# Kernel tuning notes

Measured on AMD Instinct MI355X. Metric: run time of the kernel, lower is better.

The kernel has to match this reference:

```python
import jax, jax.numpy as jnp
import numpy as np

D_MODEL = 512
INF = 1e9
TEMP = np.sqrt(D_MODEL).astype(np.float32)


def setup_inputs() -> dict:
    key = jax.random.key(0)
    kq, kk, kv, km = jax.random.split(key, 4)
    B, L, D = 64, 1024, 64  # B = batch*heads
    q = jax.random.normal(kq, (B, L, D), dtype=jnp.float32)
    k = jax.random.normal(kk, (B, L, D), dtype=jnp.float32)
    v = jax.random.normal(kv, (B, L, D), dtype=jnp.float32)
    attn_mask = jax.random.randint(km, (B, L, L), 0, 2).astype(jnp.bool_)
    return {"q": q, "k": k, "v": v, "attn_mask": attn_mask}


def reference(q, k, v, attn_mask):
    # scores: [b, len_q, len_k]
    attn = jnp.einsum('bqd,bkd->bqk', q, k) / TEMP
    attn = jnp.where(attn_mask, -INF, attn)
    attn = jax.nn.softmax(attn, axis=2)
    # dropout p=0.0 -> identity
    out = jnp.einsum('bqk,bkd->bqd', attn, v)
    return out
```

## Files before the change

kernel.cpp:

```cpp
#include <hip/hip_runtime.h>
#include <hip/hip_bf16.h>


typedef __attribute__((ext_vector_type(4))) float f32x4;
typedef __attribute__((ext_vector_type(8))) short bf16x8;
typedef __attribute__((ext_vector_type(4))) short short4v;

constexpr int B_ = 64;
constexpr int L_ = 1024;
constexpr int D_ = 64;
constexpr int QBLK = 64;
constexpr int KV = 64;
constexpr int NT_H = 8;
constexpr int STR = 72;
constexpr float SC2 = 0.06376003f;
constexpr float NEG = -1e9f;
constexpr float THR = 8.0f;

constexpr int HBUF = 64 * STR * 2;

__device__ inline short f2bf(float f) {
  __hip_bfloat16 h = __float2bfloat16(f);
  short s; __builtin_memcpy(&s, &h, 2);
  return s;
}
__device__ inline unsigned int pk2(float a, float b) {
  return (unsigned int)(unsigned short)f2bf(a)
       | ((unsigned int)(unsigned short)f2bf(b) << 16);
}

__global__ __launch_bounds__(512, 4) void attn_fwd(
    const float* __restrict__ Q, const float* __restrict__ K,
    const float* __restrict__ V, const int* __restrict__ M,
    float* __restrict__ O)
{
  __shared__ __align__(16) unsigned char smem[4 * HBUF + 512];

  const int tid  = threadIdx.x;
  const int w    = tid >> 6;
  const int half = w >> 2;
  const int w4   = w & 3;
  const int lane = tid & 63;
  const int g    = lane >> 4;
  const int c    = lane & 15;
  const int htid = tid & 255;
  const int b    = blockIdx.y;
  const int q0   = blockIdx.x * QBLK;

  short (*k_lds)[STR]  = (short(*)[STR])(smem + half * (2 * HBUF));
  short (*vt_lds)[STR] = (short(*)[STR])(smem + half * (2 * HBUF) + HBUF);

  bf16x8 qf[2];
  {
    const float* qp = Q + ((size_t)b * L_ + q0 + w4 * 16 + c) * D_ + g * 8;
#pragma unroll
    for (int ks = 0; ks < 2; ++ks) {
      f32x4 x0 = *(const f32x4*)(qp + ks * 32);
      f32x4 x1 = *(const f32x4*)(qp + ks * 32 + 4);
      bf16x8 t;
      t[0] = f2bf(x0[0]); t[1] = f2bf(x0[1]); t[2] = f2bf(x0[2]); t[3] = f2bf(x0[3]);
      t[4] = f2bf(x1[0]); t[5] = f2bf(x1[1]); t[6] = f2bf(x1[2]); t[7] = f2bf(x1[3]);
      qf[ks] = t;
    }
  }

  const float* Kb = K + (size_t)b * L_ * D_ + (size_t)half * NT_H * KV * D_;
  const float* Vb = V + (size_t)b * L_ * D_ + (size_t)half * NT_H * KV * D_;
  const int* mlane = M + (size_t)b * L_ * L_
                   + (size_t)(q0 + w4 * 16 + c) * L_ + half * (NT_H * KV) + 4 * g;

  const int vkey4 = (htid & 15) * 4;
  const int vd4   = (htid >> 4) * 4;

  auto stage = [&](int t) {
    const float* ksrc = Kb + (size_t)(t * KV) * D_;
    const float* vsrc = Vb + (size_t)(t * KV) * D_;
#pragma unroll
    for (int i = 0; i < 4; ++i) {
      const int idx = htid + i * 256;
      f32x4 kx = *(const f32x4*)(ksrc + (size_t)idx * 4);
      short4v ks4 = { f2bf(kx[0]), f2bf(kx[1]), f2bf(kx[2]), f2bf(kx[3]) };
      *(short4v*)&k_lds[idx >> 4][(idx & 15) * 4] = ks4;
    }
    f32x4 vreg[4];
#pragma unroll
    for (int i = 0; i < 4; ++i)
      vreg[i] = *(const f32x4*)(vsrc + (size_t)(vkey4 + i) * D_ + vd4);
#pragma unroll
    for (int i = 0; i < 4; ++i) {
      const int jj = (i + (htid >> 4)) & 3;
      short4v vt4 = { f2bf(vreg[0][jj]), f2bf(vreg[1][jj]),
                      f2bf(vreg[2][jj]), f2bf(vreg[3][jj]) };
      *(short4v*)&vt_lds[vd4 + jj][vkey4] = vt4;
    }
  };

  f32x4 acc[4];
#pragma unroll
  for (int i = 0; i < 4; ++i) acc[i] = (f32x4){0.f, 0.f, 0.f, 0.f};
  float m_run = -INFINITY;
  float l_run = 0.f;

  stage(0);
  __syncthreads();

  for (int t = 0; t < NT_H; ++t) {
    unsigned int mc = 0;
#pragma unroll
    for (int f = 0; f < 4; ++f) {
      const int4 lm = *(const int4*)(mlane + t * KV + f * 16);
      mc |= (lm.x != 0 ? 1u : 0u) << (f * 4 + 0);
      mc |= (lm.y != 0 ? 1u : 0u) << (f * 4 + 1);
      mc |= (lm.z != 0 ? 1u : 0u) << (f * 4 + 2);
      mc |= (lm.w != 0 ? 1u : 0u) << (f * 4 + 3);
    }

    f32x4 sc[4];
#pragma unroll
    for (int f = 0; f < 4; ++f) {
      f32x4 a = (f32x4){0.f, 0.f, 0.f, 0.f};
#pragma unroll
      for (int ks = 0; ks < 2; ++ks) {
        bf16x8 kf = *(const bf16x8*)&k_lds[f * 16 + c][ks * 32 + g * 8];
        a = __builtin_amdgcn_mfma_f32_16x16x32_bf16(kf, qf[ks], a, 0, 0, 0);
      }
      sc[f] = a;
    }

#pragma unroll
    for (int f = 0; f < 4; ++f)
#pragma unroll
      for (int r = 0; r < 4; ++r)
        sc[f][r] = ((mc >> (f * 4 + r)) & 1u) ? NEG : sc[f][r] * SC2;

    float xl = sc[0][0];
#pragma unroll
    for (int f = 0; f < 4; ++f)
#pragma unroll
      for (int r = 0; r < 4; ++r) xl = fmaxf(xl, sc[f][r]);
    if (!__all(xl <= m_run + THR)) {
      float x = fmaxf(xl, __shfl_xor(xl, 16, 64));
      x = fmaxf(x, __shfl_xor(x, 32, 64));
      const float m_new = fmaxf(m_run, x);
      const float alpha = exp2f(m_run - m_new);
      l_run *= alpha;
      float ar[4];
#pragma unroll
      for (int r = 0; r < 4; ++r)
        ar[r] = __shfl(alpha, (lane & 48) | (g * 4 + r), 64);
#pragma unroll
      for (int fd = 0; fd < 4; ++fd)
#pragma unroll
        for (int r = 0; r < 4; ++r) acc[fd][r] *= ar[r];
      m_run = m_new;
    }
    float s = 0.f;
#pragma unroll
    for (int f = 0; f < 4; ++f)
#pragma unroll
      for (int r = 0; r < 4; ++r) {
        const float p = exp2f(sc[f][r] - m_run);
        sc[f][r] = p;
        s += p;
      }
    l_run += s;

    unsigned int pd[4][2];
#pragma unroll
    for (int f = 0; f < 4; ++f) {
      pd[f][0] = pk2(sc[f][0], sc[f][1]);
      pd[f][1] = pk2(sc[f][2], sc[f][3]);
    }
    const int rev2 = ((g & 1) << 1) | (g >> 1);
    const int srcA = rev2 * 16 + c;
    const int srcB = srcA ^ 16;
    const bool podd = (g & 1) != 0;
    const bool gh   = (g >= 2);
    unsigned int d0[4], d1[4];
#pragma unroll
    for (int k = 0; k < 4; ++k) {
      const int fb = 2 * (k >> 1);
      const int hh = k & 1;
      const unsigned int pubA = podd ? pd[fb + 1][hh] : pd[fb + 0][hh];
      const unsigned int pubB = podd ? pd[fb + 0][hh] : pd[fb + 1][hh];
      const unsigned int rvA = (unsigned int)__shfl((int)pubA, srcA, 64);
      const unsigned int rvB = (unsigned int)__shfl((int)pubB, srcB, 64);
      if (k < 2) {
        if (gh) { d0[2 + hh] = rvA; d0[hh] = rvB; }
        else    { d0[hh] = rvA; d0[2 + hh] = rvB; }
      } else {
        if (gh) { d1[2 + hh] = rvA; d1[hh] = rvB; }
        else    { d1[hh] = rvA; d1[2 + hh] = rvB; }
      }
    }
    bf16x8 pa0, pa1;
    __builtin_memcpy(&pa0, d0, 16);
    __builtin_memcpy(&pa1, d1, 16);

#pragma unroll
    for (int fd = 0; fd < 4; ++fd) {
      bf16x8 vb0 = *(const bf16x8*)&vt_lds[fd * 16 + c][g * 8];
      acc[fd] = __builtin_amdgcn_mfma_f32_16x16x32_bf16(pa0, vb0, acc[fd], 0, 0, 0);
      bf16x8 vb1 = *(const bf16x8*)&vt_lds[fd * 16 + c][32 + g * 8];
      acc[fd] = __builtin_amdgcn_mfma_f32_16x16x32_bf16(pa1, vb1, acc[fd], 0, 0, 0);
    }

    if (t + 1 < NT_H) {
      __syncthreads();
      stage(t + 1);
      __syncthreads();
    }
  }

  float l = l_run;
  l += __shfl_xor(l, 16, 64);
  l += __shfl_xor(l, 32, 64);

  __syncthreads();
  f32x4* cacc = (f32x4*)smem;
  float2* cml = (float2*)(smem + 4 * HBUF);
  if (half == 1) {
#pragma unroll
    for (int fd = 0; fd < 4; ++fd)
      cacc[(w4 * 64 + lane) * 4 + fd] = acc[fd];
    if (g == 0) cml[w4 * 16 + c] = make_float2(m_run, l);
  }
  __syncthreads();
  if (half == 0) {
    const float2 mlB = cml[w4 * 16 + c];
    const float Mx = fmaxf(m_run, mlB.x);
    const float wA = exp2f(m_run - Mx);
    const float wB = exp2f(mlB.x - Mx);
    const float li = 1.0f / (wA * l + wB * mlB.y);
    float arA[4], arB[4], lr[4];
#pragma unroll
    for (int r = 0; r < 4; ++r) {
      const int src = (lane & 48) | (g * 4 + r);
      arA[r] = __shfl(wA, src, 64);
      arB[r] = __shfl(wB, src, 64);
      lr[r]  = __shfl(li, src, 64);
    }
    float* orow = O + ((size_t)b * L_ + q0 + w4 * 16 + g * 4) * D_;
#pragma unroll
    for (int fd = 0; fd < 4; ++fd) {
      const f32x4 ab = cacc[(w4 * 64 + lane) * 4 + fd];
#pragma unroll
      for (int r = 0; r < 4; ++r)
        orow[(size_t)r * D_ + fd * 16 + c] =
            (arA[r] * acc[fd][r] + arB[r] * ab[r]) * lr[r];
    }
  }
}

extern "C" void kernel_launch(void* const* d_in, const int* in_sizes, int n_in,
                              void* d_out, int out_size, void* d_ws, size_t ws_size,
                              hipStream_t stream) {
  const float* q = (const float*)d_in[0];
  const float* k = (const float*)d_in[1];
  const float* v = (const float*)d_in[2];
  const int* m = (const int*)d_in[3];
  float* o = (float*)d_out;
  dim3 grid(L_ / QBLK, B_);
  attn_fwd<<<grid, 512, 0, stream>>>(q, k, v, m, o);
}
```

Before: 117.2 us.

## Double-buffer K/V in LDS and prefetch tiles and mask into registers

Doubles the LDS buffers so each half-block loads the next K/V tile from global into registers before computing the current tile, then writes it to the alternate buffer. This removes one barrier per iteration. Mask loads are prefetched two tiles ahead, and the loop is unrolled by two so the mask registers can alternate. In exchange, LDS usage doubles, register pressure grows, and the occupancy hint in launch bounds drops from 4 to 2 blocks, which may reduce latency hiding across waves.

```diff
diff --git a/kernel.cpp b/kernel.cpp
--- a/kernel.cpp
+++ b/kernel.cpp
@@ -17,7 +17,8 @@
 constexpr float NEG = -1e9f;
 constexpr float THR = 8.0f;
 
-constexpr int HBUF = 64 * STR * 2;
+constexpr int HBUF    = 64 * STR * 2;
+constexpr int HALFREG = 4 * HBUF;
 
 __device__ inline short f2bf(float f) {
   __hip_bfloat16 h = __float2bfloat16(f);
@@ -29,12 +30,12 @@
        | ((unsigned int)(unsigned short)f2bf(b) << 16);
 }
 
-__global__ __launch_bounds__(512, 4) void attn_fwd(
+__global__ __launch_bounds__(512, 2) void attn_fwd(
     const float* __restrict__ Q, const float* __restrict__ K,
     const float* __restrict__ V, const int* __restrict__ M,
     float* __restrict__ O)
 {
-  __shared__ __align__(16) unsigned char smem[4 * HBUF + 512];
+  __shared__ __align__(16) unsigned char smem[2 * HALFREG + 512];
 
   const int tid  = threadIdx.x;
   const int w    = tid >> 6;
@@ -47,8 +48,12 @@
   const int b    = blockIdx.y;
   const int q0   = blockIdx.x * QBLK;
 
-  short (*k_lds)[STR]  = (short(*)[STR])(smem + half * (2 * HBUF));
-  short (*vt_lds)[STR] = (short(*)[STR])(smem + half * (2 * HBUF) + HBUF);
+  auto k_base  = [&](int buf) {
+    return (short(*)[STR])(smem + half * HALFREG + buf * (2 * HBUF));
+  };
+  auto vt_base = [&](int buf) {
+    return (short(*)[STR])(smem + half * HALFREG + buf * (2 * HBUF) + HBUF);
+  };
 
   bf16x8 qf[2];
   {
@@ -72,27 +77,48 @@
   const int vkey4 = (htid & 15) * 4;
   const int vd4   = (htid >> 4) * 4;
 
-  auto stage = [&](int t) {
+  f32x4 kreg[4], vreg[4];
+  int4  mr0[4], mr1[4];
+
+  auto load_kv = [&](int t) {
     const float* ksrc = Kb + (size_t)(t * KV) * D_;
     const float* vsrc = Vb + (size_t)(t * KV) * D_;
 #pragma unroll
     for (int i = 0; i < 4; ++i) {
+      kreg[i] = *(const f32x4*)(ksrc + (size_t)(htid + i * 256) * 4);
+      vreg[i] = *(const f32x4*)(vsrc + (size_t)(vkey4 + i) * D_ + vd4);
+    }
+  };
+  auto load_m = [&](int t, int4 (&mr)[4]) {
+#pragma unroll
+    for (int f = 0; f < 4; ++f)
+      mr[f] = *(const int4*)(mlane + t * KV + f * 16);
+  };
+  auto write_kv = [&](int buf) {
+    short (*kl)[STR]  = k_base(buf);
+    short (*vtl)[STR] = vt_base(buf);
+#pragma unroll
+    for (int i = 0; i < 4; ++i) {
       const int idx = htid + i * 256;
-      f32x4 kx = *(const f32x4*)(ksrc + (size_t)idx * 4);
-      short4v ks4 = { f2bf(kx[0]), f2bf(kx[1]), f2bf(kx[2]), f2bf(kx[3]) };
-      *(short4v*)&k_lds[idx >> 4][(idx & 15) * 4] = ks4;
-    }
-    f32x4 vreg[4];
-#pragma unroll
-    for (int i = 0; i < 4; ++i)
-      vreg[i] = *(const f32x4*)(vsrc + (size_t)(vkey4 + i) * D_ + vd4);
-#pragma unroll
-    for (int i = 0; i < 4; ++i) {
+      short4v ks4 = { f2bf(kreg[i][0]), f2bf(kreg[i][1]),
+                      f2bf(kreg[i][2]), f2bf(kreg[i][3]) };
+      *(short4v*)&kl[idx >> 4][(idx & 15) * 4] = ks4;
       const int jj = (i + (htid >> 4)) & 3;
       short4v vt4 = { f2bf(vreg[0][jj]), f2bf(vreg[1][jj]),
                       f2bf(vreg[2][jj]), f2bf(vreg[3][jj]) };
-      *(short4v*)&vt_lds[vd4 + jj][vkey4] = vt4;
-    }
+      *(short4v*)&vtl[vd4 + jj][vkey4] = vt4;
+    }
+  };
+  auto packm = [&](const int4 (&lm)[4]) {
+    unsigned int mp = 0;
+#pragma unroll
+    for (int f = 0; f < 4; ++f) {
+      mp |= (lm[f].x != 0 ? 1u : 0u) << (f * 4 + 0);
+      mp |= (lm[f].y != 0 ? 1u : 0u) << (f * 4 + 1);
+      mp |= (lm[f].z != 0 ? 1u : 0u) << (f * 4 + 2);
+      mp |= (lm[f].w != 0 ? 1u : 0u) << (f * 4 + 3);
+    }
+    return mp;
   };
 
   f32x4 acc[4];
@@ -101,27 +127,30 @@
   float m_run = -INFINITY;
   float l_run = 0.f;
 
-  stage(0);
+  load_kv(0);
+  write_kv(0);
+  load_m(0, mr0);
+  load_m(1, mr1);
+  __builtin_amdgcn_sched_barrier(0);
   __syncthreads();
 
-  for (int t = 0; t < NT_H; ++t) {
-    unsigned int mc = 0;
-#pragma unroll
-    for (int f = 0; f < 4; ++f) {
-      const int4 lm = *(const int4*)(mlane + t * KV + f * 16);
-      mc |= (lm.x != 0 ? 1u : 0u) << (f * 4 + 0);
-      mc |= (lm.y != 0 ? 1u : 0u) << (f * 4 + 1);
-      mc |= (lm.z != 0 ? 1u : 0u) << (f * 4 + 2);
-      mc |= (lm.w != 0 ? 1u : 0u) << (f * 4 + 3);
-    }
-
+  auto body = [&](int t, int4 (&mr)[4]) {
+    const int cur = t & 1;
+    const bool has_next = (t + 1 < NT_H);
+    if (has_next) load_kv(t + 1);
+    const unsigned int mc = packm(mr);
+    if (t + 2 < NT_H) load_m(t + 2, mr);
+    __builtin_amdgcn_sched_barrier(0);
+
+    short (*kl)[STR]  = k_base(cur);
+    short (*vtl)[STR] = vt_base(cur);
     f32x4 sc[4];
 #pragma unroll
     for (int f = 0; f < 4; ++f) {
       f32x4 a = (f32x4){0.f, 0.f, 0.f, 0.f};
 #pragma unroll
       for (int ks = 0; ks < 2; ++ks) {
-        bf16x8 kf = *(const bf16x8*)&k_lds[f * 16 + c][ks * 32 + g * 8];
+        bf16x8 kf = *(const bf16x8*)&kl[f * 16 + c][ks * 32 + g * 8];
         a = __builtin_amdgcn_mfma_f32_16x16x32_bf16(kf, qf[ks], a, 0, 0, 0);
       }
       sc[f] = a;
@@ -199,17 +228,21 @@
 
 #pragma unroll
     for (int fd = 0; fd < 4; ++fd) {
-      bf16x8 vb0 = *(const bf16x8*)&vt_lds[fd * 16 + c][g * 8];
+      bf16x8 vb0 = *(const bf16x8*)&vtl[fd * 16 + c][g * 8];
       acc[fd] = __builtin_amdgcn_mfma_f32_16x16x32_bf16(pa0, vb0, acc[fd], 0, 0, 0);
-      bf16x8 vb1 = *(const bf16x8*)&vt_lds[fd * 16 + c][32 + g * 8];
+      bf16x8 vb1 = *(const bf16x8*)&vtl[fd * 16 + c][32 + g * 8];
       acc[fd] = __builtin_amdgcn_mfma_f32_16x16x32_bf16(pa1, vb1, acc[fd], 0, 0, 0);
     }
 
-    if (t + 1 < NT_H) {
+    if (has_next) {
+      write_kv(cur ^ 1);
       __syncthreads();
-      stage(t + 1);
-      __syncthreads();
-    }
+    }
+  };
+
+  for (int tt = 0; tt < NT_H; tt += 2) {
+    body(tt,     mr0);
+    body(tt + 1, mr1);
   }
 
   float l = l_run;
@@ -218,7 +251,7 @@
 
   __syncthreads();
   f32x4* cacc = (f32x4*)smem;
-  float2* cml = (float2*)(smem + 4 * HBUF);
+  float2* cml = (float2*)(smem + 2 * HALFREG);
   if (half == 1) {
 #pragma unroll
     for (int fd = 0; fd < 4; ++fd)
```

New measurement: 175.4 us. +49.7%, slower.

## Prefetch next K/V tile and mask into registers to overlap with compute

Applied to the files above, without the earlier changes.

Splits staging into global load, bf16 conversion and LDS write, and issues the loads for tile t+1 (K, V and the mask) at the start of iteration t. The global latency is then hidden behind the QK MFMAs and softmax instead of sitting between barriers. Scheduling barriers pin the load placement. Launch bounds drop from 4 to 2 blocks per SM to make room for the extra live registers, which may cut occupancy.

```diff
diff --git a/kernel.cpp b/kernel.cpp
--- a/kernel.cpp
+++ b/kernel.cpp
@@ -17,7 +17,8 @@
 constexpr float NEG = -1e9f;
 constexpr float THR = 8.0f;
 
-constexpr int HBUF = 64 * STR * 2;
+constexpr int HBUF     = 64 * STR * 2;
+constexpr int HALF_LDS = 2 * HBUF;
 
 __device__ inline short f2bf(float f) {
   __hip_bfloat16 h = __float2bfloat16(f);
@@ -29,12 +30,12 @@
        | ((unsigned int)(unsigned short)f2bf(b) << 16);
 }
 
-__global__ __launch_bounds__(512, 4) void attn_fwd(
+__global__ __launch_bounds__(512, 2) void attn_fwd(
     const float* __restrict__ Q, const float* __restrict__ K,
     const float* __restrict__ V, const int* __restrict__ M,
     float* __restrict__ O)
 {
-  __shared__ __align__(16) unsigned char smem[4 * HBUF + 512];
+  __shared__ __align__(16) unsigned char smem[2 * HALF_LDS + 512];
 
   const int tid  = threadIdx.x;
   const int w    = tid >> 6;
@@ -47,8 +48,8 @@
   const int b    = blockIdx.y;
   const int q0   = blockIdx.x * QBLK;
 
-  short (*k_lds)[STR]  = (short(*)[STR])(smem + half * (2 * HBUF));
-  short (*vt_lds)[STR] = (short(*)[STR])(smem + half * (2 * HBUF) + HBUF);
+  short (*k_lds)[STR]  = (short(*)[STR])(smem + half * HALF_LDS);
+  short (*vt_lds)[STR] = (short(*)[STR])(smem + half * HALF_LDS + HBUF);
 
   bf16x8 qf[2];
   {
@@ -72,26 +73,41 @@
   const int vkey4 = (htid & 15) * 4;
   const int vd4   = (htid >> 4) * 4;
 
-  auto stage = [&](int t) {
+  f32x4   kreg[4], vreg[4];
+  short4v ksh[4], vsh[4];
+  int4    mr[4];
+
+  auto load_kv = [&](int t) {
     const float* ksrc = Kb + (size_t)(t * KV) * D_;
     const float* vsrc = Vb + (size_t)(t * KV) * D_;
 #pragma unroll
     for (int i = 0; i < 4; ++i) {
+      kreg[i] = *(const f32x4*)(ksrc + (size_t)(htid + i * 256) * 4);
+      vreg[i] = *(const f32x4*)(vsrc + (size_t)(vkey4 + i) * D_ + vd4);
+    }
+  };
+  auto load_m = [&](int t) {
+#pragma unroll
+    for (int f = 0; f < 4; ++f)
+      mr[f] = *(const int4*)(mlane + t * KV + f * 16);
+  };
+  auto cvt_kv = [&]() {
+#pragma unroll
+    for (int i = 0; i < 4; ++i) {
+      ksh[i] = short4v{ f2bf(kreg[i][0]), f2bf(kreg[i][1]),
+                        f2bf(kreg[i][2]), f2bf(kreg[i][3]) };
+      const int jj = (i + (htid >> 4)) & 3;
+      vsh[i] = short4v{ f2bf(vreg[0][jj]), f2bf(vreg[1][jj]),
+                        f2bf(vreg[2][jj]), f2bf(vreg[3][jj]) };
+    }
+  };
+  auto write_kv = [&]() {
+#pragma unroll
+    for (int i = 0; i < 4; ++i) {
       const int idx = htid + i * 256;
-      f32x4 kx = *(const f32x4*)(ksrc + (size_t)idx * 4);
-      short4v ks4 = { f2bf(kx[0]), f2bf(kx[1]), f2bf(kx[2]), f2bf(kx[3]) };
-      *(short4v*)&k_lds[idx >> 4][(idx & 15) * 4] = ks4;
-    }
-    f32x4 vreg[4];
-#pragma unroll
-    for (int i = 0; i < 4; ++i)
-      vreg[i] = *(const f32x4*)(vsrc + (size_t)(vkey4 + i) * D_ + vd4);
-#pragma unroll
-    for (int i = 0; i < 4; ++i) {
+      *(short4v*)&k_lds[idx >> 4][(idx & 15) * 4] = ksh[i];
       const int jj = (i + (htid >> 4)) & 3;
-      short4v vt4 = { f2bf(vreg[0][jj]), f2bf(vreg[1][jj]),
-                      f2bf(vreg[2][jj]), f2bf(vreg[3][jj]) };
-      *(short4v*)&vt_lds[vd4 + jj][vkey4] = vt4;
+      *(short4v*)&vt_lds[vd4 + jj][vkey4] = vsh[i];
     }
   };
 
@@ -101,19 +117,16 @@
   float m_run = -INFINITY;
   float l_run = 0.f;
 
-  stage(0);
+  load_kv(0);
+  load_m(0);
+  cvt_kv();
+  write_kv();
   __syncthreads();
 
   for (int t = 0; t < NT_H; ++t) {
-    unsigned int mc = 0;
-#pragma unroll
-    for (int f = 0; f < 4; ++f) {
-      const int4 lm = *(const int4*)(mlane + t * KV + f * 16);
-      mc |= (lm.x != 0 ? 1u : 0u) << (f * 4 + 0);
-      mc |= (lm.y != 0 ? 1u : 0u) << (f * 4 + 1);
-      mc |= (lm.z != 0 ? 1u : 0u) << (f * 4 + 2);
-      mc |= (lm.w != 0 ? 1u : 0u) << (f * 4 + 3);
-    }
+    const bool has_next = (t + 1 < NT_H);
+    if (has_next) load_kv(t + 1);
+    __builtin_amdgcn_sched_barrier(0);
 
     f32x4 sc[4];
 #pragma unroll
@@ -128,10 +141,15 @@
     }
 
 #pragma unroll
-    for (int f = 0; f < 4; ++f)
-#pragma unroll
-      for (int r = 0; r < 4; ++r)
-        sc[f][r] = ((mc >> (f * 4 + r)) & 1u) ? NEG : sc[f][r] * SC2;
+    for (int f = 0; f < 4; ++f) {
+      const int4 mm = mr[f];
+      sc[f][0] = mm.x ? NEG : sc[f][0] * SC2;
+      sc[f][1] = mm.y ? NEG : sc[f][1] * SC2;
+      sc[f][2] = mm.z ? NEG : sc[f][2] * SC2;
+      sc[f][3] = mm.w ? NEG : sc[f][3] * SC2;
+    }
+    if (has_next) load_m(t + 1);
+    __builtin_amdgcn_sched_barrier(0);
 
     float xl = sc[0][0];
 #pragma unroll
@@ -205,9 +223,10 @@
       acc[fd] = __builtin_amdgcn_mfma_f32_16x16x32_bf16(pa1, vb1, acc[fd], 0, 0, 0);
     }
 
-    if (t + 1 < NT_H) {
+    if (has_next) {
+      cvt_kv();
       __syncthreads();
-      stage(t + 1);
+      write_kv();
       __syncthreads();
     }
   }
@@ -218,7 +237,7 @@
 
   __syncthreads();
   f32x4* cacc = (f32x4*)smem;
-  float2* cml = (float2*)(smem + 4 * HBUF);
+  float2* cml = (float2*)(smem + 2 * HALF_LDS);
   if (half == 1) {
 #pragma unroll
     for (int fd = 0; fd < 4; ++fd)
```

Result: slower. 147.3 us (+25.7%).
